# Kernel optimization log

Measured on AMD Instinct MI355X. Metric: run time of the kernel, lower is better.

## Reference

```python
import jax, jax.numpy as jnp
import numpy as np
import math

A = 256            # n_agents == batch rows (epymarl stacks agents along batch)
B = A
OBS = 512          # obs_shape = (input_shape - n_actions) // 2
NA = 64            # n_actions
MSG = 2048         # messages_shape (divisible by A)
H = 1024           # hidden_dim
T = 3              # trajectory_length
TAU = OBS + NA
VD = MSG // A      # per-agent message dim


def setup_inputs() -> dict:
    key = jax.random.key(0)
    keys = iter(jax.random.split(key, 40))
    def lin(o, i):
        w = jax.random.normal(next(keys), (o, i), jnp.float32) * (i ** -0.5)
        return w, jnp.zeros((o,), jnp.float32)
    d = {}
    d["inputs"] = jax.random.normal(next(keys), (B, 2 * OBS + NA + MSG), jnp.float32)
    d["hidden_state"] = jax.random.normal(next(keys), (B, 3 * H), jnp.float32) * 0.1
    for name, o, i in [("pi_fc1", H, OBS + MSG), ("pi_fc2", NA, H),
                       ("fa_fc1", H, OBS), ("fa_fc2", (A - 1) * NA, H),
                       ("fo_fc1", H, NA * A + OBS), ("fo_fc2", OBS, H),
                       ("am_qs", H, MSG), ("am_ks", H, TAU), ("am_vs", VD, TAU)]:
        d[name + "_w"], d[name + "_b"] = lin(o, i)
    for name in ["pi_rnn", "fa_rnn", "fo_rnn"]:
        d[name + "_wih"], d[name + "_bih"] = lin(3 * H, H)
        d[name + "_whh"], d[name + "_bhh"] = lin(3 * H, H)
    return d


def _gru(x, h, wih, whh, bih, bhh):
    gi = x @ wih.T + bih
    gh = h @ whh.T + bhh
    ir, iz, i_n = jnp.split(gi, 3, -1)
    hr, hz, h_n = jnp.split(gh, 3, -1)
    r = jax.nn.sigmoid(ir + hr)
    z = jax.nn.sigmoid(iz + hz)
    n = jnp.tanh(i_n + r * h_n)
    return (1.0 - z) * n + z * h


def reference(inputs, hidden_state,
              pi_fc1_w, pi_fc1_b, pi_fc2_w, pi_fc2_b,
              pi_rnn_wih, pi_rnn_whh, pi_rnn_bih, pi_rnn_bhh,
              fa_fc1_w, fa_fc1_b, fa_fc2_w, fa_fc2_b,
              fa_rnn_wih, fa_rnn_whh, fa_rnn_bih, fa_rnn_bhh,
              fo_fc1_w, fo_fc1_b, fo_fc2_w, fo_fc2_b,
              fo_rnn_wih, fo_rnn_whh, fo_rnn_bih, fo_rnn_bhh,
              am_qs_w, am_qs_b, am_ks_w, am_ks_b, am_vs_w, am_vs_b):
    sg = jax.lax.stop_gradient
    lin = lambda x, w, b: x @ w.T + b
    h_fa = hidden_state[:, :H]
    h_fo = hidden_state[:, H:2 * H]
    h_pi0 = hidden_state[:, -H:]
    obs = inputs[:, :OBS]
    prev_obs = inputs[:, OBS:2 * OBS]
    prev_act = sg(inputs[:, 2 * OBS:2 * OBS + NA])   # .detach() in torch
    prev_msg = inputs[:, -MSG:]

    def pi(o, m, h):
        x = jax.nn.relu(lin(jnp.concatenate([o, m], -1), pi_fc1_w, pi_fc1_b))
        h2 = _gru(x, h, pi_rnn_wih, pi_rnn_whh, pi_rnn_bih, pi_rnn_bhh)
        return lin(h2, pi_fc2_w, pi_fc2_b), h2

    # ---- ImaginedTrajectory rollout (fixed small T, python loop is structural) ----
    o, a, h_pi = prev_obs, prev_act, h_pi0
    observations, actions = [o], [a]
    for _ in range(T - 1):
        x = jax.nn.relu(lin(o, fa_fc1_w, fa_fc1_b))
        h_fa = _gru(x, h_fa, fa_rnn_wih, fa_rnn_whh, fa_rnn_bih, fa_rnn_bhh)
        q = lin(h_fa, fa_fc2_w, fa_fc2_b)                       # [B,(A-1)*NA]
        qs = jax.nn.softmax(q.reshape(B, A - 1, NA), -1)
        # torch stack(qs_out).reshape(orig): scrambles (A-1,B) order, kept faithfully
        fa = jnp.transpose(qs, (1, 0, 2)).reshape(B, (A - 1) * NA)
        x2 = jax.nn.relu(lin(jnp.concatenate([fa, a, o], -1), fo_fc1_w, fo_fc1_b))
        h_fo = _gru(x2, h_fo, fo_rnn_wih, fo_rnn_whh, fo_rnn_bih, fo_rnn_bhh)
        nxt_o = lin(h_fo, fo_fc2_w, fo_fc2_b)
        nxt_a, h_pi = pi(sg(o), sg(prev_msg), sg(h_pi))         # forward_pi detaches inputs
        o, a = nxt_o, nxt_a
        observations.append(o)
        actions.append(a)
    taus = jnp.stack([jnp.concatenate([observations[t], actions[t]], -1)
                      for t in range(T)])                        # [T,B,TAU]

    # ---- AttentionMechanism: batched equivalent of the per-agent python loops ----
    # k rows are indexed j*n_agents + i with batch == n_agents, i.e. k[t, b] here.
    qv = lin(prev_msg, am_qs_w, am_qs_b)                         # [B,H]
    kk = jnp.einsum('tbi,hi->tbh', taus, am_ks_w) + am_ks_b      # [T,B,H]
    vv = jnp.einsum('tbi,vi->tbv', taus, am_vs_w) + am_vs_b      # [T,B,VD]
    alpha = jax.nn.softmax(jnp.einsum('bh,tbh->bt', qv, kk) / math.sqrt(H), -1)
    new_message = jnp.einsum('bt,tbv->bv', alpha, vv)            # [B,VD]

    # cat([msg]*A, 0).reshape(B,-1): each agent receives all agents' messages
    pi_msg = jnp.tile(new_message, (A, 1)).reshape(B, -1)        # [B,MSG]
    action, h_pi_f = pi(obs, pi_msg, h_pi0)                      # uses ORIGINAL h_pi slice
    h_out = jnp.concatenate([h_fa, h_fo, h_pi_f], -1)            # [B,3H]
    q_out = jnp.concatenate([new_message, action], -1)           # [B,VD+NA]
    return q_out, h_out
```

## Files before the change

kernel.cpp:

```cpp
#include <hip/hip_runtime.h>
#include <hip/hip_bf16.h>
#include <math.h>

#define OBS 512
#define MSG 2048
#define TAU 576
#define TAUP 640
#define QN 16320
#define X2W 16896
#define INW 3136
#define PIW 2560

typedef short short8v __attribute__((ext_vector_type(8)));
typedef float f32x4 __attribute__((ext_vector_type(4)));

__device__ inline unsigned short bfbits(float x) {
  __hip_bfloat16 h = __float2bfloat16(x);
  return *reinterpret_cast<unsigned short*>(&h);
}

__device__ inline void gload16(const void* g, void* l) {
  __builtin_amdgcn_global_load_lds((__attribute__((address_space(1))) void*)(g),
                                   (__attribute__((address_space(3))) void*)(l), 16, 0, 0);
}

struct MMSet {
  const __hip_bfloat16* A;
  const float* W;
  const float* bias;
  float* C;
  __hip_bfloat16* Cb;
  int lda, ldw, ldc, ldcb;
};

template<int BM, int ACT, bool ATOMIC, bool DUAL>
__global__ __launch_bounds__(512)
void k_mm(MMSet s0, MMSet s1, int kSteps)
{
  constexpr int AREP = BM / 64;
  __shared__ __hip_bfloat16 As[2][BM * 64];
  __shared__ __hip_bfloat16 Bs[2][64 * 64];
  const MMSet S = (DUAL && blockIdx.z) ? s1 : s0;
  const int tid = threadIdx.x;
  const int lane = tid & 63;
  const int wid = tid >> 6;
  const int m0 = blockIdx.y * BM;
  const int n0 = blockIdx.x * 64;
  const size_t k0 = ATOMIC ? (size_t)blockIdx.z * kSteps * 64 : 0;

  const __hip_bfloat16* Ab = S.A + (size_t)m0 * S.lda + k0;
  const float* Bb = S.W + (size_t)n0 * S.ldw + k0;

  int arow[AREP], acol[AREP], adst[AREP];
#pragma unroll
  for (int r = 0; r < AREP; ++r) {
    int chunk = r * 512 + tid;
    arow[r] = chunk >> 3;
    acol[r] = ((chunk & 7) ^ (arow[r] & 7)) * 8;
    adst[r] = chunk * 8;
  }
  int brow[2], bcol[2], bdst[2];
#pragma unroll
  for (int r = 0; r < 2; ++r) {
    int c = r * 512 + tid;
    brow[r] = c >> 4;
    int g = (c & 15) >> 1, half = c & 1;
    bcol[r] = (c & 15) * 4;
    bdst[r] = brow[r] * 64 + ((g ^ (brow[r] & 7)) << 3) + half * 4;
  }

  const int wr = wid >> 1, wc = wid & 1;
  const int fr = lane & 15, q = lane >> 4;
  const int xm = fr & 7;

  f32x4 acc[AREP][2] = {};
  float4 bv0, bv1;

  auto stageA = [&](int buf, int kt) {
#pragma unroll
    for (int r = 0; r < AREP; ++r)
      gload16(Ab + (size_t)arow[r] * S.lda + kt + acol[r], &As[buf][adst[r]]);
  };
  auto loadB = [&](int kt) {
    bv0 = *(const float4*)(Bb + (size_t)brow[0] * S.ldw + kt + bcol[0]);
    bv1 = *(const float4*)(Bb + (size_t)brow[1] * S.ldw + kt + bcol[1]);
  };
  auto writeB = [&](int buf) {
    ushort4 w0, w1;
    w0.x = bfbits(bv0.x); w0.y = bfbits(bv0.y); w0.z = bfbits(bv0.z); w0.w = bfbits(bv0.w);
    w1.x = bfbits(bv1.x); w1.y = bfbits(bv1.y); w1.z = bfbits(bv1.z); w1.w = bfbits(bv1.w);
    *(ushort4*)&Bs[buf][bdst[0]] = w0;
    *(ushort4*)&Bs[buf][bdst[1]] = w1;
  };

  stageA(0, 0);
  loadB(0);
  writeB(0);
  __syncthreads();

  for (int t = 0; t < kSteps; ++t) {
    const int buf = t & 1;
    if (t + 1 < kSteps) {
      stageA(buf ^ 1, (t + 1) * 64);
      loadB((t + 1) * 64);
    }
    const __hip_bfloat16* Ac = As[buf];
    const __hip_bfloat16* Bc = Bs[buf];
#pragma unroll
    for (int ks = 0; ks < 2; ++ks) {
      const int cc = ks * 4 + q;
      const int co = ((cc ^ xm) << 3);
      short8v b0 = *(const short8v*)&Bc[(wc * 32 +  0 + fr) * 64 + co];
      short8v b1 = *(const short8v*)&Bc[(wc * 32 + 16 + fr) * 64 + co];
#pragma unroll
      for (int i = 0; i < AREP; ++i) {
        short8v a = *(const short8v*)&Ac[(wr * (AREP * 16) + i * 16 + fr) * 64 + co];
        acc[i][0] = __builtin_amdgcn_mfma_f32_16x16x32_bf16(a, b0, acc[i][0], 0, 0, 0);
        acc[i][1] = __builtin_amdgcn_mfma_f32_16x16x32_bf16(a, b1, acc[i][1], 0, 0, 0);
      }
    }
    if (t + 1 < kSteps) writeB(buf ^ 1);
    __syncthreads();
  }

#pragma unroll
  for (int i = 0; i < AREP; ++i) {
    const int mb = m0 + wr * (AREP * 16) + i * 16 + q * 4;
#pragma unroll
    for (int j = 0; j < 2; ++j) {
      const int n = n0 + wc * 32 + j * 16 + fr;
      if (ATOMIC) {
#pragma unroll
        for (int v = 0; v < 4; ++v)
          atomicAdd(&S.C[(size_t)(mb + v) * S.ldc + n], acc[i][j][v]);
      } else {
        const float bb = S.bias[n];
#pragma unroll
        for (int v = 0; v < 4; ++v) {
          float val = acc[i][j][v] + bb;
          if (ACT) val = fmaxf(val, 0.f);
          if (S.C)  S.C[(size_t)(mb + v) * S.ldc + n] = val;
          if (S.Cb) S.Cb[(size_t)(mb + v) * S.ldcb + n] = __float2bfloat16(val);
        }
      }
    }
  }
}

__global__ __launch_bounds__(256)
void k_init(const float* __restrict__ in, const float* __restrict__ hid,
            float* __restrict__ h32a, float* __restrict__ h32o, float* __restrict__ h32p,
            __hip_bfloat16* __restrict__ hba, __hip_bfloat16* __restrict__ hbo,
            __hip_bfloat16* __restrict__ hbp, __hip_bfloat16* __restrict__ hbp0,
            __hip_bfloat16* __restrict__ taus, __hip_bfloat16* __restrict__ msgb)
{
  const int bx = blockIdx.x;
  if (bx < 3072) {
    int idx = bx * 256 + threadIdx.x;
    int b = idx / 3072, c = idx % 3072;
    float v = hid[idx];
    __hip_bfloat16 hb = __float2bfloat16(v);
    int j = c & 1023;
    if (c < 1024)      { h32a[b * 1024 + j] = v; hba[b * 1024 + j] = hb; }
    else if (c < 2048) { h32o[b * 1024 + j] = v; hbo[b * 1024 + j] = hb; }
    else               { h32p[b * 1024 + j] = v; hbp[b * 1024 + j] = hb; hbp0[b * 1024 + j] = hb; }
  } else if (bx < 3072 + 1920) {
    int idx = (bx - 3072) * 256 + threadIdx.x;
    int t = idx / (256 * TAUP);
    int r = (idx / TAUP) % 256;
    int c = idx % TAUP;
    float v = 0.f;
    if (t == 0 && c < TAU)
      v = (c < OBS) ? in[(size_t)r * INW + OBS + c]
                    : in[(size_t)r * INW + 2 * OBS + (c - OBS)];
    taus[idx] = __float2bfloat16(v);
  } else {
    int idx = (bx - 3072 - 1920) * 256 + threadIdx.x;
    int b = idx >> 11, c = idx & 2047;
    msgb[idx] = __float2bfloat16(in[(size_t)b * INW + 1088 + c]);
  }
}

__global__ __launch_bounds__(256)
void k_gru(const float* __restrict__ gi, const float* __restrict__ gh,
           const float* __restrict__ hs, int ldsrc,
           float* __restrict__ hd, int lddst, __hip_bfloat16* __restrict__ hb)
{
  int idx = blockIdx.x * 256 + threadIdx.x;
  int b = idx >> 10, j = idx & 1023;
  float ir = gi[b * 3072 + j];
  float iz = gi[b * 3072 + 1024 + j];
  float in_ = gi[b * 3072 + 2048 + j];
  float hr = gh[b * 3072 + j];
  float hz = gh[b * 3072 + 1024 + j];
  float hn = gh[b * 3072 + 2048 + j];
  float r = 1.f / (1.f + expf(-(ir + hr)));
  float z = 1.f / (1.f + expf(-(iz + hz)));
  float n = tanhf(in_ + r * hn);
  float h = hs[(size_t)b * ldsrc + j];
  float o = (1.f - z) * n + z * h;
  hd[(size_t)b * lddst + j] = o;
  hb[idx] = __float2bfloat16(o);
}

__global__ __launch_bounds__(256)
void k_softmax_scatter(const __hip_bfloat16* __restrict__ q, __hip_bfloat16* __restrict__ x2)
{
  int wid = blockIdx.x * 4 + (threadIdx.x >> 6);
  int lane = threadIdx.x & 63;
  int b = wid / 255, p = wid % 255;
  float v = __bfloat162float(q[(size_t)b * QN + p * 64 + lane]);
  float m = v;
#pragma unroll
  for (int s = 32; s; s >>= 1) m = fmaxf(m, __shfl_xor(m, s));
  float e = expf(v - m);
  float sum = e;
#pragma unroll
  for (int s = 32; s; s >>= 1) sum += __shfl_xor(sum, s);
  float r = e / sum;
  int flat = p * 16384 + b * 64 + lane;
  int bp = flat / QN;
  int j = flat - bp * QN;
  x2[(size_t)bp * X2W + j] = __float2bfloat16(r);
}

__global__ __launch_bounds__(256)
void k_x2_tail(const __hip_bfloat16* __restrict__ taus_t, __hip_bfloat16* __restrict__ x2)
{
  int idx = blockIdx.x * 256 + threadIdx.x;
  int b = idx / TAU, c = idx % TAU;
  if (c < 64)
    x2[(size_t)b * X2W + QN + c] = taus_t[(size_t)b * TAUP + OBS + c];
  else
    x2[(size_t)b * X2W + QN + 64 + (c - 64)] = taus_t[(size_t)b * TAUP + (c - 64)];
}

__global__ __launch_bounds__(256)
void k_concat_pi_loop(const __hip_bfloat16* __restrict__ taus_t,
                      const __hip_bfloat16* __restrict__ msg,
                      __hip_bfloat16* __restrict__ piin)
{
  int idx = blockIdx.x * 256 + threadIdx.x;
  int b = idx / PIW, c = idx % PIW;
  piin[idx] = (c < OBS) ? taus_t[(size_t)b * TAUP + c] : msg[b * MSG + (c - OBS)];
}

__global__ __launch_bounds__(256)
void k_concat_pi_final(const float* __restrict__ in, const float* __restrict__ nm,
                       __hip_bfloat16* __restrict__ piin)
{
  int idx = blockIdx.x * 256 + threadIdx.x;
  int b = idx / PIW, c = idx % PIW;
  float v = (c < OBS) ? in[(size_t)b * INW + c] : nm[c - OBS];
  piin[idx] = __float2bfloat16(v);
}

__global__ __launch_bounds__(256)
void k_fill_bias(float* __restrict__ C, const float* __restrict__ bias)
{
  int idx = blockIdx.x * 256 + threadIdx.x;
  C[idx] = bias[idx & 1023];
}

__global__ __launch_bounds__(256)
void k_relu_cvt(const float* __restrict__ s, __hip_bfloat16* __restrict__ d)
{
  int idx = blockIdx.x * 256 + threadIdx.x;
  d[idx] = __float2bfloat16(fmaxf(s[idx], 0.f));
}

__global__ __launch_bounds__(64)
void k_vv(const __hip_bfloat16* __restrict__ taus, const float* __restrict__ w,
          const float* __restrict__ bias, float* __restrict__ vv)
{
  int row = blockIdx.x;
  int lane = threadIdx.x;
  const __hip_bfloat16* tr = taus + (size_t)row * TAUP;
  for (int v = 0; v < 8; ++v) {
    float s = 0.f;
    for (int k = lane; k < TAU; k += 64) s += __bfloat162float(tr[k]) * w[v * TAU + k];
#pragma unroll
    for (int d = 32; d; d >>= 1) s += __shfl_xor(s, d);
    if (lane == 0) vv[row * 8 + v] = s + bias[v];
  }
}

__global__ __launch_bounds__(64)
void k_attn(const float* __restrict__ qv, const float* __restrict__ kk,
            const float* __restrict__ vv, float* __restrict__ nm,
            float* __restrict__ out_q)
{
  int b = blockIdx.x;
  int lane = threadIdx.x;
  const float* qb = qv + (size_t)b * 1024;
  float s[3];
#pragma unroll
  for (int t = 0; t < 3; ++t) {
    const float* kb = kk + (size_t)(t * 256 + b) * 1024;
    float acc = 0.f;
    for (int h = lane; h < 1024; h += 64) acc += qb[h] * kb[h];
#pragma unroll
    for (int d = 32; d; d >>= 1) acc += __shfl_xor(acc, d);
    s[t] = acc * (1.f / 32.f);
  }
  float m = fmaxf(s[0], fmaxf(s[1], s[2]));
  float e0 = expf(s[0] - m), e1 = expf(s[1] - m), e2 = expf(s[2] - m);
  float inv = 1.f / (e0 + e1 + e2);
  float a0 = e0 * inv, a1 = e1 * inv, a2 = e2 * inv;
  if (lane < 8) {
    float v = a0 * vv[(0 * 256 + b) * 8 + lane]
            + a1 * vv[(1 * 256 + b) * 8 + lane]
            + a2 * vv[(2 * 256 + b) * 8 + lane];
    nm[b * 8 + lane] = v;
    out_q[b * 72 + lane] = v;
  }
}

__global__ __launch_bounds__(256)
void k_copy_hout(const float* __restrict__ hfa, const float* __restrict__ hfo,
                 float* __restrict__ hout)
{
  int idx = blockIdx.x * 256 + threadIdx.x;
  int b = idx / 2048, c = idx % 2048;
  float v = (c < 1024) ? hfa[b * 1024 + c] : hfo[b * 1024 + (c - 1024)];
  hout[(size_t)b * 3072 + c] = v;
}

extern "C" void kernel_launch(void* const* d_in, const int* in_sizes, int n_in,
                              void* d_out_v, int out_size, void* d_ws, size_t ws_size,
                              hipStream_t stream)
{
  const float* inputs   = (const float*)d_in[0];
  const float* hidden   = (const float*)d_in[1];
  const float* pi_fc1_w = (const float*)d_in[2];
  const float* pi_fc1_b = (const float*)d_in[3];
  const float* pi_fc2_w = (const float*)d_in[4];
  const float* pi_fc2_b = (const float*)d_in[5];
  const float* fa_fc1_w = (const float*)d_in[6];
  const float* fa_fc1_b = (const float*)d_in[7];
  const float* fa_fc2_w = (const float*)d_in[8];
  const float* fa_fc2_b = (const float*)d_in[9];
  const float* fo_fc1_w = (const float*)d_in[10];
  const float* fo_fc1_b = (const float*)d_in[11];
  const float* fo_fc2_w = (const float*)d_in[12];
  const float* fo_fc2_b = (const float*)d_in[13];
  const float* am_qs_w  = (const float*)d_in[14];
  const float* am_qs_b  = (const float*)d_in[15];
  const float* am_ks_w  = (const float*)d_in[16];
  const float* am_ks_b  = (const float*)d_in[17];
  const float* am_vs_w  = (const float*)d_in[18];
  const float* am_vs_b  = (const float*)d_in[19];
  const float* pi_wih   = (const float*)d_in[20];
  const float* pi_bih   = (const float*)d_in[21];
  const float* pi_whh   = (const float*)d_in[22];
  const float* pi_bhh   = (const float*)d_in[23];
  const float* fa_wih   = (const float*)d_in[24];
  const float* fa_bih   = (const float*)d_in[25];
  const float* fa_whh   = (const float*)d_in[26];
  const float* fa_bhh   = (const float*)d_in[27];
  const float* fo_wih   = (const float*)d_in[28];
  const float* fo_bih   = (const float*)d_in[29];
  const float* fo_whh   = (const float*)d_in[30];
  const float* fo_bhh   = (const float*)d_in[31];

  float* out = (float*)d_out_v;
  char* p = (char*)d_ws;
  auto alloc = [&](size_t bytes) { void* r = p; p += (bytes + 255) & ~(size_t)255; return r; };
  typedef __hip_bfloat16 bf;

  bf* HFAB = (bf*)alloc((size_t)256 * 1024 * 2);
  bf* HFOB = (bf*)alloc((size_t)256 * 1024 * 2);
  bf* HPIB = (bf*)alloc((size_t)256 * 1024 * 2);
  bf* HPI0B = (bf*)alloc((size_t)256 * 1024 * 2);
  bf* XBUFB = (bf*)alloc((size_t)256 * 1024 * 2);
  bf* TAUSB = (bf*)alloc((size_t)3 * 256 * TAUP * 2);
  bf* X2B  = (bf*)alloc((size_t)256 * X2W * 2);
  bf* PIINB = (bf*)alloc((size_t)256 * PIW * 2);
  bf* MSGB = (bf*)alloc((size_t)256 * MSG * 2);
  bf* QBUFB = (bf*)alloc((size_t)256 * QN * 2);
  float* HFA32 = (float*)alloc((size_t)256 * 1024 * 4);
  float* HFO32 = (float*)alloc((size_t)256 * 1024 * 4);
  float* HPI32 = (float*)alloc((size_t)256 * 1024 * 4);
  float* XBUF32 = (float*)alloc((size_t)256 * 1024 * 4);
  float* GI = (float*)alloc((size_t)256 * 3072 * 4);
  float* GH = (float*)alloc((size_t)256 * 3072 * 4);
  float* QV = (float*)alloc((size_t)256 * 1024 * 4);
  float* KK = (float*)alloc((size_t)768 * 1024 * 4);
  float* VV = (float*)alloc((size_t)768 * 8 * 4);
  float* NM = (float*)alloc((size_t)2048 * 4);

  auto mset = [&](const bf* A, int lda, const float* W, int ldw, const float* bias,
                  float* C, int ldc, bf* Cb, int ldcb) {
    MMSet s; s.A = A; s.W = W; s.bias = bias; s.C = C; s.Cb = Cb;
    s.lda = lda; s.ldw = ldw; s.ldc = ldc; s.ldcb = ldcb; return s;
  };
  auto mm256 = [&](MMSet a, int M, int N, int K) {
    dim3 g(N / 64, M / 256, 1);
    k_mm<256, 0, false, false><<<g, 512, 0, stream>>>(a, a, K / 64);
  };
  auto mm128 = [&](MMSet a, int M, int N, int K) {
    dim3 g(N / 64, M / 128, 1);
    k_mm<128, 0, false, false><<<g, 512, 0, stream>>>(a, a, K / 64);
  };
  auto mm64 = [&](MMSet a, int N, int K, int act) {
    dim3 g(N / 64, 4, 1);
    if (act) k_mm<64, 1, false, false><<<g, 512, 0, stream>>>(a, a, K / 64);
    else     k_mm<64, 0, false, false><<<g, 512, 0, stream>>>(a, a, K / 64);
  };
  auto mmDual = [&](MMSet a, MMSet b, int N, int K) {
    dim3 g(N / 64, 2, 2);
    k_mm<128, 0, false, true><<<g, 512, 0, stream>>>(a, b, K / 64);
  };

  k_init<<<3072 + 1920 + 2048, 256, 0, stream>>>(inputs, hidden,
      HFA32, HFO32, HPI32, HFAB, HFOB, HPIB, HPI0B, TAUSB, MSGB);

  for (int t = 0; t < 2; ++t) {
    bf* taus_t = TAUSB + (size_t)t * 256 * TAUP;
    bf* taus_n = TAUSB + (size_t)(t + 1) * 256 * TAUP;
    mm64(mset(taus_t, TAUP, fa_fc1_w, 512, fa_fc1_b, nullptr, 0, XBUFB, 1024), 1024, 512, 1);
    mmDual(mset(XBUFB, 1024, fa_wih, 1024, fa_bih, GI, 3072, nullptr, 0),
           mset(HFAB, 1024, fa_whh, 1024, fa_bhh, GH, 3072, nullptr, 0), 3072, 1024);
    k_gru<<<1024, 256, 0, stream>>>(GI, GH, HFA32, 1024, HFA32, 1024, HFAB);
    mm256(mset(HFAB, 1024, fa_fc2_w, 1024, fa_fc2_b, nullptr, 0, QBUFB, QN), 256, QN, 1024);
    k_x2_tail<<<576, 256, 0, stream>>>(taus_t, X2B);
    k_softmax_scatter<<<16320, 256, 0, stream>>>(QBUFB, X2B);
    k_fill_bias<<<1024, 256, 0, stream>>>(XBUF32, fo_fc1_b);
    {
      dim3 g(16, 1, 12);
      MMSet s = mset(X2B, X2W, fo_fc1_w, X2W, fo_fc1_b, XBUF32, 1024, nullptr, 0);
      k_mm<256, 0, true, false><<<g, 512, 0, stream>>>(s, s, 22);
    }
    k_relu_cvt<<<1024, 256, 0, stream>>>(XBUF32, XBUFB);
    mmDual(mset(XBUFB, 1024, fo_wih, 1024, fo_bih, GI, 3072, nullptr, 0),
           mset(HFOB, 1024, fo_whh, 1024, fo_bhh, GH, 3072, nullptr, 0), 3072, 1024);
    k_gru<<<1024, 256, 0, stream>>>(GI, GH, HFO32, 1024, HFO32, 1024, HFOB);
    mm64(mset(HFOB, 1024, fo_fc2_w, 1024, fo_fc2_b, nullptr, 0, taus_n, TAUP), 512, 1024, 0);
    k_concat_pi_loop<<<2560, 256, 0, stream>>>(taus_t, MSGB, PIINB);
    mm64(mset(PIINB, PIW, pi_fc1_w, PIW, pi_fc1_b, nullptr, 0, XBUFB, 1024), 1024, PIW, 1);
    mmDual(mset(XBUFB, 1024, pi_wih, 1024, pi_bih, GI, 3072, nullptr, 0),
           mset(HPIB, 1024, pi_whh, 1024, pi_bhh, GH, 3072, nullptr, 0), 3072, 1024);
    k_gru<<<1024, 256, 0, stream>>>(GI, GH, HPI32, 1024, HPI32, 1024, HPIB);
    mm64(mset(HPIB, 1024, pi_fc2_w, 1024, pi_fc2_b, nullptr, 0, taus_n + OBS, TAUP), 64, 1024, 0);
  }

  mm64(mset(MSGB, MSG, am_qs_w, MSG, am_qs_b, QV, 1024, nullptr, 0), 1024, 2048, 0);
  mm128(mset(TAUSB, TAUP, am_ks_w, TAU, am_ks_b, KK, 1024, nullptr, 0), 768, 1024, TAU);
  k_vv<<<768, 64, 0, stream>>>(TAUSB, am_vs_w, am_vs_b, VV);
  k_attn<<<256, 64, 0, stream>>>(QV, KK, VV, NM, out);

  k_concat_pi_final<<<2560, 256, 0, stream>>>(inputs, NM, PIINB);
  mm64(mset(PIINB, PIW, pi_fc1_w, PIW, pi_fc1_b, nullptr, 0, XBUFB, 1024), 1024, PIW, 1);
  mmDual(mset(XBUFB, 1024, pi_wih, 1024, pi_bih, GI, 3072, nullptr, 0),
         mset(HPI0B, 1024, pi_whh, 1024, pi_bhh, GH, 3072, nullptr, 0), 3072, 1024);
  k_gru<<<1024, 256, 0, stream>>>(GI, GH, hidden + 2048, 3072,
                                  out + 256 * 72 + 2048, 3072, HPIB);
  mm64(mset(HPIB, 1024, pi_fc2_w, 1024, pi_fc2_b, out + 8, 72, nullptr, 0), 64, 1024, 0);
  k_copy_hout<<<2048, 256, 0, stream>>>(HFA32, HFO32, out + 256 * 72);
  (void)in_sizes; (void)n_in; (void)out_size; (void)ws_size;
}
```

Measured before the change: 611.9 us.

## Triple-buffer GEMM pipeline, enlarge tiles, fold fo_fc1 bias fill into init

The GEMM main loop moves from a double-buffered to a triple-buffered LDS pipeline. Loads run two k-steps ahead, with explicit lgkmcnt waits, barriers and raised wave priority around the MFMA block, to hide global load latency. Several launches switch to larger M tiles (the dual GRU GEMMs to BM=256, pi_fc1 and am_qs to BM=128, am_ks to BM=256), which cuts weight re-reads but leaves fewer blocks in the grid. The separate bias-fill kernel for the atomic fo_fc1 accumulation is dropped and both per-step buffers are pre-filled in the init kernel, at the cost of one extra 1 MB buffer and 50% more LDS per block.

After: 801.7 us. +31.0%, slower.

```diff
diff --git a/kernel.cpp b/kernel.cpp
--- a/kernel.cpp
+++ b/kernel.cpp
@@ -24,6 +24,13 @@
                                    (__attribute__((address_space(3))) void*)(l), 16, 0, 0);
 }
 
+__device__ inline void bar_lgkm() {
+  __builtin_amdgcn_sched_barrier(0);
+  asm volatile("s_waitcnt lgkmcnt(0)" ::: "memory");
+  __builtin_amdgcn_s_barrier();
+  __builtin_amdgcn_sched_barrier(0);
+}
+
 struct MMSet {
   const __hip_bfloat16* A;
   const float* W;
@@ -38,8 +45,8 @@
 void k_mm(MMSet s0, MMSet s1, int kSteps)
 {
   constexpr int AREP = BM / 64;
-  __shared__ __hip_bfloat16 As[2][BM * 64];
-  __shared__ __hip_bfloat16 Bs[2][64 * 64];
+  __shared__ __hip_bfloat16 As[3][BM * 64];
+  __shared__ __hip_bfloat16 Bs[3][64 * 64];
   const MMSet S = (DUAL && blockIdx.z) ? s1 : s0;
   const int tid = threadIdx.x;
   const int lane = tid & 63;
@@ -74,38 +81,53 @@
   const int xm = fr & 7;
 
   f32x4 acc[AREP][2] = {};
-  float4 bv0, bv1;
+  float4 p0a, p0b, p1a, p1b;
 
   auto stageA = [&](int buf, int kt) {
 #pragma unroll
     for (int r = 0; r < AREP; ++r)
       gload16(Ab + (size_t)arow[r] * S.lda + kt + acol[r], &As[buf][adst[r]]);
   };
-  auto loadB = [&](int kt) {
-    bv0 = *(const float4*)(Bb + (size_t)brow[0] * S.ldw + kt + bcol[0]);
-    bv1 = *(const float4*)(Bb + (size_t)brow[1] * S.ldw + kt + bcol[1]);
-  };
-  auto writeB = [&](int buf) {
+  auto loadB0 = [&](int kt) {
+    p0a = *(const float4*)(Bb + (size_t)brow[0] * S.ldw + kt + bcol[0]);
+    p0b = *(const float4*)(Bb + (size_t)brow[1] * S.ldw + kt + bcol[1]);
+  };
+  auto loadB1 = [&](int kt) {
+    p1a = *(const float4*)(Bb + (size_t)brow[0] * S.ldw + kt + bcol[0]);
+    p1b = *(const float4*)(Bb + (size_t)brow[1] * S.ldw + kt + bcol[1]);
+  };
+  auto writeB0 = [&](int buf) {
     ushort4 w0, w1;
-    w0.x = bfbits(bv0.x); w0.y = bfbits(bv0.y); w0.z = bfbits(bv0.z); w0.w = bfbits(bv0.w);
-    w1.x = bfbits(bv1.x); w1.y = bfbits(bv1.y); w1.z = bfbits(bv1.z); w1.w = bfbits(bv1.w);
+    w0.x = bfbits(p0a.x); w0.y = bfbits(p0a.y); w0.z = bfbits(p0a.z); w0.w = bfbits(p0a.w);
+    w1.x = bfbits(p0b.x); w1.y = bfbits(p0b.y); w1.z = bfbits(p0b.z); w1.w = bfbits(p0b.w);
     *(ushort4*)&Bs[buf][bdst[0]] = w0;
     *(ushort4*)&Bs[buf][bdst[1]] = w1;
   };
-
-  stageA(0, 0);
-  loadB(0);
-  writeB(0);
-  __syncthreads();
+  auto writeB1 = [&](int buf) {
+    ushort4 w0, w1;
+    w0.x = bfbits(p1a.x); w0.y = bfbits(p1a.y); w0.z = bfbits(p1a.z); w0.w = bfbits(p1a.w);
+    w1.x = bfbits(p1b.x); w1.y = bfbits(p1b.y); w1.z = bfbits(p1b.z); w1.w = bfbits(p1b.w);
+    *(ushort4*)&Bs[buf][bdst[0]] = w0;
+    *(ushort4*)&Bs[buf][bdst[1]] = w1;
+  };
+
+  stageA(0, 0); loadB0(0);
+  if (kSteps > 1) { stageA(1, 64); loadB1(64); }
+  writeB0(0);
 
   for (int t = 0; t < kSteps; ++t) {
-    const int buf = t & 1;
+    bar_lgkm();
+    if (t + 2 < kSteps) {
+      stageA((t + 2) % 3, (t + 2) * 64);
+      if (t & 1) loadB1((t + 2) * 64); else loadB0((t + 2) * 64);
+    }
     if (t + 1 < kSteps) {
-      stageA(buf ^ 1, (t + 1) * 64);
-      loadB((t + 1) * 64);
+      if (t & 1) writeB0((t + 1) % 3); else writeB1((t + 1) % 3);
     }
-    const __hip_bfloat16* Ac = As[buf];
-    const __hip_bfloat16* Bc = Bs[buf];
+    bar_lgkm();
+    const __hip_bfloat16* Ac = As[t % 3];
+    const __hip_bfloat16* Bc = Bs[t % 3];
+    __builtin_amdgcn_s_setprio(1);
 #pragma unroll
     for (int ks = 0; ks < 2; ++ks) {
       const int cc = ks * 4 + q;
@@ -119,8 +141,7 @@
         acc[i][1] = __builtin_amdgcn_mfma_f32_16x16x32_bf16(a, b1, acc[i][1], 0, 0, 0);
       }
     }
-    if (t + 1 < kSteps) writeB(buf ^ 1);
-    __syncthreads();
+    __builtin_amdgcn_s_setprio(0);
   }
 
 #pragma unroll
@@ -152,7 +173,8 @@
             float* __restrict__ h32a, float* __restrict__ h32o, float* __restrict__ h32p,
             __hip_bfloat16* __restrict__ hba, __hip_bfloat16* __restrict__ hbo,
             __hip_bfloat16* __restrict__ hbp, __hip_bfloat16* __restrict__ hbp0,
-            __hip_bfloat16* __restrict__ taus, __hip_bfloat16* __restrict__ msgb)
+            __hip_bfloat16* __restrict__ taus, __hip_bfloat16* __restrict__ msgb,
+            const float* __restrict__ fo1b, float* __restrict__ xb0, float* __restrict__ xb1)
 {
   const int bx = blockIdx.x;
   if (bx < 3072) {
@@ -174,10 +196,14 @@
       v = (c < OBS) ? in[(size_t)r * INW + OBS + c]
                     : in[(size_t)r * INW + 2 * OBS + (c - OBS)];
     taus[idx] = __float2bfloat16(v);
-  } else {
+  } else if (bx < 3072 + 1920 + 2048) {
     int idx = (bx - 3072 - 1920) * 256 + threadIdx.x;
     int b = idx >> 11, c = idx & 2047;
     msgb[idx] = __float2bfloat16(in[(size_t)b * INW + 1088 + c]);
+  } else {
+    int idx = (bx - 3072 - 1920 - 2048) * 256 + threadIdx.x;
+    float v = fo1b[idx & 1023];
+    xb0[idx] = v; xb1[idx] = v;
   }
 }
 
@@ -253,13 +279,6 @@
   int b = idx / PIW, c = idx % PIW;
   float v = (c < OBS) ? in[(size_t)b * INW + c] : nm[c - OBS];
   piin[idx] = __float2bfloat16(v);
-}
-
-__global__ __launch_bounds__(256)
-void k_fill_bias(float* __restrict__ C, const float* __restrict__ bias)
-{
-  int idx = blockIdx.x * 256 + threadIdx.x;
-  C[idx] = bias[idx & 1023];
 }
 
 __global__ __launch_bounds__(256)
@@ -381,7 +400,8 @@
   float* HFA32 = (float*)alloc((size_t)256 * 1024 * 4);
   float* HFO32 = (float*)alloc((size_t)256 * 1024 * 4);
   float* HPI32 = (float*)alloc((size_t)256 * 1024 * 4);
-  float* XBUF32 = (float*)alloc((size_t)256 * 1024 * 4);
+  float* XBUF32A = (float*)alloc((size_t)256 * 1024 * 4);
+  float* XBUF32B = (float*)alloc((size_t)256 * 1024 * 4);
   float* GI = (float*)alloc((size_t)256 * 3072 * 4);
   float* GH = (float*)alloc((size_t)256 * 3072 * 4);
   float* QV = (float*)alloc((size_t)256 * 1024 * 4);
@@ -398,9 +418,10 @@
     dim3 g(N / 64, M / 256, 1);
     k_mm<256, 0, false, false><<<g, 512, 0, stream>>>(a, a, K / 64);
   };
-  auto mm128 = [&](MMSet a, int M, int N, int K) {
+  auto mm128 = [&](MMSet a, int M, int N, int K, int act) {
     dim3 g(N / 64, M / 128, 1);
-    k_mm<128, 0, false, false><<<g, 512, 0, stream>>>(a, a, K / 64);
+    if (act) k_mm<128, 1, false, false><<<g, 512, 0, stream>>>(a, a, K / 64);
+    else     k_mm<128, 0, false, false><<<g, 512, 0, stream>>>(a, a, K / 64);
   };
   auto mm64 = [&](MMSet a, int N, int K, int act) {
     dim3 g(N / 64, 4, 1);
@@ -408,16 +429,18 @@
     else     k_mm<64, 0, false, false><<<g, 512, 0, stream>>>(a, a, K / 64);
   };
   auto mmDual = [&](MMSet a, MMSet b, int N, int K) {
-    dim3 g(N / 64, 2, 2);
-    k_mm<128, 0, false, true><<<g, 512, 0, stream>>>(a, b, K / 64);
-  };
-
-  k_init<<<3072 + 1920 + 2048, 256, 0, stream>>>(inputs, hidden,
-      HFA32, HFO32, HPI32, HFAB, HFOB, HPIB, HPI0B, TAUSB, MSGB);
+    dim3 g(N / 64, 1, 2);
+    k_mm<256, 0, false, true><<<g, 512, 0, stream>>>(a, b, K / 64);
+  };
+
+  k_init<<<3072 + 1920 + 2048 + 1024, 256, 0, stream>>>(inputs, hidden,
+      HFA32, HFO32, HPI32, HFAB, HFOB, HPIB, HPI0B, TAUSB, MSGB,
+      fo_fc1_b, XBUF32A, XBUF32B);
 
   for (int t = 0; t < 2; ++t) {
     bf* taus_t = TAUSB + (size_t)t * 256 * TAUP;
     bf* taus_n = TAUSB + (size_t)(t + 1) * 256 * TAUP;
+    float* xb32 = t ? XBUF32B : XBUF32A;
     mm64(mset(taus_t, TAUP, fa_fc1_w, 512, fa_fc1_b, nullptr, 0, XBUFB, 1024), 1024, 512, 1);
     mmDual(mset(XBUFB, 1024, fa_wih, 1024, fa_bih, GI, 3072, nullptr, 0),
            mset(HFAB, 1024, fa_whh, 1024, fa_bhh, GH, 3072, nullptr, 0), 3072, 1024);
@@ -425,32 +448,31 @@
     mm256(mset(HFAB, 1024, fa_fc2_w, 1024, fa_fc2_b, nullptr, 0, QBUFB, QN), 256, QN, 1024);
     k_x2_tail<<<576, 256, 0, stream>>>(taus_t, X2B);
     k_softmax_scatter<<<16320, 256, 0, stream>>>(QBUFB, X2B);
-    k_fill_bias<<<1024, 256, 0, stream>>>(XBUF32, fo_fc1_b);
     {
       dim3 g(16, 1, 12);
-      MMSet s = mset(X2B, X2W, fo_fc1_w, X2W, fo_fc1_b, XBUF32, 1024, nullptr, 0);
+      MMSet s = mset(X2B, X2W, fo_fc1_w, X2W, fo_fc1_b, xb32, 1024, nullptr, 0);
       k_mm<256, 0, true, false><<<g, 512, 0, stream>>>(s, s, 22);
     }
-    k_relu_cvt<<<1024, 256, 0, stream>>>(XBUF32, XBUFB);
+    k_relu_cvt<<<1024, 256, 0, stream>>>(xb32, XBUFB);
     mmDual(mset(XBUFB, 1024, fo_wih, 1024, fo_bih, GI, 3072, nullptr, 0),
            mset(HFOB, 1024, fo_whh, 1024, fo_bhh, GH, 3072, nullptr, 0), 3072, 1024);
     k_gru<<<1024, 256, 0, stream>>>(GI, GH, HFO32, 1024, HFO32, 1024, HFOB);
     mm64(mset(HFOB, 1024, fo_fc2_w, 1024, fo_fc2_b, nullptr, 0, taus_n, TAUP), 512, 1024, 0);
     k_concat_pi_loop<<<2560, 256, 0, stream>>>(taus_t, MSGB, PIINB);
-    mm64(mset(PIINB, PIW, pi_fc1_w, PIW, pi_fc1_b, nullptr, 0, XBUFB, 1024), 1024, PIW, 1);
+    mm128(mset(PIINB, PIW, pi_fc1_w, PIW, pi_fc1_b, nullptr, 0, XBUFB, 1024), 256, 1024, PIW, 1);
     mmDual(mset(XBUFB, 1024, pi_wih, 1024, pi_bih, GI, 3072, nullptr, 0),
            mset(HPIB, 1024, pi_whh, 1024, pi_bhh, GH, 3072, nullptr, 0), 3072, 1024);
     k_gru<<<1024, 256, 0, stream>>>(GI, GH, HPI32, 1024, HPI32, 1024, HPIB);
     mm64(mset(HPIB, 1024, pi_fc2_w, 1024, pi_fc2_b, nullptr, 0, taus_n + OBS, TAUP), 64, 1024, 0);
   }
 
-  mm64(mset(MSGB, MSG, am_qs_w, MSG, am_qs_b, QV, 1024, nullptr, 0), 1024, 2048, 0);
-  mm128(mset(TAUSB, TAUP, am_ks_w, TAU, am_ks_b, KK, 1024, nullptr, 0), 768, 1024, TAU);
+  mm128(mset(MSGB, MSG, am_qs_w, MSG, am_qs_b, QV, 1024, nullptr, 0), 256, 1024, 2048, 0);
+  mm256(mset(TAUSB, TAUP, am_ks_w, TAU, am_ks_b, KK, 1024, nullptr, 0), 768, 1024, TAU);
   k_vv<<<768, 64, 0, stream>>>(TAUSB, am_vs_w, am_vs_b, VV);
   k_attn<<<256, 64, 0, stream>>>(QV, KK, VV, NM, out);
 
   k_concat_pi_final<<<2560, 256, 0, stream>>>(inputs, NM, PIINB);
-  mm64(mset(PIINB, PIW, pi_fc1_w, PIW, pi_fc1_b, nullptr, 0, XBUFB, 1024), 1024, PIW, 1);
+  mm128(mset(PIINB, PIW, pi_fc1_w, PIW, pi_fc1_b, nullptr, 0, XBUFB, 1024), 256, 1024, PIW, 1);
   mmDual(mset(XBUFB, 1024, pi_wih, 1024, pi_bih, GI, 3072, nullptr, 0),
          mset(HPI0B, 1024, pi_whh, 1024, pi_bhh, GH, 3072, nullptr, 0), 3072, 1024);
   k_gru<<<1024, 256, 0, stream>>>(GI, GH, hidden + 2048, 3072,
```

## Use uniform 64x64 GEMM tiles, split-K pi_fc1, and fold bias fills into init

Applied to the files above, without the earlier changes.

Replaces the variable-BM 512-thread GEMM kernel with a single 64x64-tile, 256-thread kernel so every GEMM launches more blocks for the small M=256 problems. The pi_fc1 GEMMs now use split-K with atomic accumulation into bias-prefilled fp32 buffers, followed by a ReLU/convert pass. The separate bias-fill kernels are folded into the init kernel, using distinct buffers per use. This trades more blocks and atomics, plus more reloads of A and weight tiles, for better CU occupancy on the skinny matmuls.

After: 637.0 us. +4.1%, slower.

```diff
diff --git a/kernel.cpp b/kernel.cpp
--- a/kernel.cpp
+++ b/kernel.cpp
@@ -13,10 +13,17 @@
 
 typedef short short8v __attribute__((ext_vector_type(8)));
 typedef float f32x4 __attribute__((ext_vector_type(4)));
+typedef __hip_bfloat16 bf;
 
 __device__ inline unsigned short bfbits(float x) {
-  __hip_bfloat16 h = __float2bfloat16(x);
+  bf h = __float2bfloat16(x);
   return *reinterpret_cast<unsigned short*>(&h);
+}
+
+__device__ inline ushort4 cvtf4(float4 v) {
+  ushort4 r;
+  r.x = bfbits(v.x); r.y = bfbits(v.y); r.z = bfbits(v.z); r.w = bfbits(v.w);
+  return r;
 }
 
 __device__ inline void gload16(const void* g, void* l) {
@@ -25,44 +32,43 @@
 }
 
 struct MMSet {
-  const __hip_bfloat16* A;
+  const bf* A;
   const float* W;
   const float* bias;
   float* C;
-  __hip_bfloat16* Cb;
+  bf* Cb;
   int lda, ldw, ldc, ldcb;
 };
 
-template<int BM, int ACT, bool ATOMIC, bool DUAL>
-__global__ __launch_bounds__(512)
+template<int ACT, bool ATOMIC, bool DUAL>
+__global__ __launch_bounds__(256)
 void k_mm(MMSet s0, MMSet s1, int kSteps)
 {
-  constexpr int AREP = BM / 64;
-  __shared__ __hip_bfloat16 As[2][BM * 64];
-  __shared__ __hip_bfloat16 Bs[2][64 * 64];
+  __shared__ bf As[2][64 * 64];
+  __shared__ bf Bs[2][64 * 64];
   const MMSet S = (DUAL && blockIdx.z) ? s1 : s0;
   const int tid = threadIdx.x;
   const int lane = tid & 63;
   const int wid = tid >> 6;
-  const int m0 = blockIdx.y * BM;
+  const int m0 = blockIdx.y * 64;
   const int n0 = blockIdx.x * 64;
   const size_t k0 = ATOMIC ? (size_t)blockIdx.z * kSteps * 64 : 0;
 
-  const __hip_bfloat16* Ab = S.A + (size_t)m0 * S.lda + k0;
+  const bf* Ab = S.A + (size_t)m0 * S.lda + k0;
   const float* Bb = S.W + (size_t)n0 * S.ldw + k0;
 
-  int arow[AREP], acol[AREP], adst[AREP];
-#pragma unroll
-  for (int r = 0; r < AREP; ++r) {
-    int chunk = r * 512 + tid;
+  int arow[2], acol[2], adst[2];
+#pragma unroll
+  for (int r = 0; r < 2; ++r) {
+    int chunk = r * 256 + tid;
     arow[r] = chunk >> 3;
     acol[r] = ((chunk & 7) ^ (arow[r] & 7)) * 8;
     adst[r] = chunk * 8;
   }
-  int brow[2], bcol[2], bdst[2];
-#pragma unroll
-  for (int r = 0; r < 2; ++r) {
-    int c = r * 512 + tid;
+  int brow[4], bcol[4], bdst[4];
+#pragma unroll
+  for (int r = 0; r < 4; ++r) {
+    int c = r * 256 + tid;
     brow[r] = c >> 4;
     int g = (c & 15) >> 1, half = c & 1;
     bcol[r] = (c & 15) * 4;
@@ -73,24 +79,25 @@
   const int fr = lane & 15, q = lane >> 4;
   const int xm = fr & 7;
 
-  f32x4 acc[AREP][2] = {};
-  float4 bv0, bv1;
+  f32x4 acc00 = {}, acc01 = {}, acc10 = {}, acc11 = {};
+  float4 w0, w1, w2, w3;
 
   auto stageA = [&](int buf, int kt) {
 #pragma unroll
-    for (int r = 0; r < AREP; ++r)
+    for (int r = 0; r < 2; ++r)
       gload16(Ab + (size_t)arow[r] * S.lda + kt + acol[r], &As[buf][adst[r]]);
   };
   auto loadB = [&](int kt) {
-    bv0 = *(const float4*)(Bb + (size_t)brow[0] * S.ldw + kt + bcol[0]);
-    bv1 = *(const float4*)(Bb + (size_t)brow[1] * S.ldw + kt + bcol[1]);
+    w0 = *(const float4*)(Bb + (size_t)brow[0] * S.ldw + kt + bcol[0]);
+    w1 = *(const float4*)(Bb + (size_t)brow[1] * S.ldw + kt + bcol[1]);
+    w2 = *(const float4*)(Bb + (size_t)brow[2] * S.ldw + kt + bcol[2]);
+    w3 = *(const float4*)(Bb + (size_t)brow[3] * S.ldw + kt + bcol[3]);
   };
   auto writeB = [&](int buf) {
-    ushort4 w0, w1;
-    w0.x = bfbits(bv0.x); w0.y = bfbits(bv0.y); w0.z = bfbits(bv0.z); w0.w = bfbits(bv0.w);
-    w1.x = bfbits(bv1.x); w1.y = bfbits(bv1.y); w1.z = bfbits(bv1.z); w1.w = bfbits(bv1.w);
-    *(ushort4*)&Bs[buf][bdst[0]] = w0;
-    *(ushort4*)&Bs[buf][bdst[1]] = w1;
+    *(ushort4*)&Bs[buf][bdst[0]] = cvtf4(w0);
+    *(ushort4*)&Bs[buf][bdst[1]] = cvtf4(w1);
+    *(ushort4*)&Bs[buf][bdst[2]] = cvtf4(w2);
+    *(ushort4*)&Bs[buf][bdst[3]] = cvtf4(w3);
   };
 
   stageA(0, 0);
@@ -104,44 +111,56 @@
       stageA(buf ^ 1, (t + 1) * 64);
       loadB((t + 1) * 64);
     }
-    const __hip_bfloat16* Ac = As[buf];
-    const __hip_bfloat16* Bc = Bs[buf];
+    const bf* Ac = As[buf];
+    const bf* Bc = Bs[buf];
 #pragma unroll
     for (int ks = 0; ks < 2; ++ks) {
       const int cc = ks * 4 + q;
       const int co = ((cc ^ xm) << 3);
+      short8v a0 = *(const short8v*)&Ac[(wr * 32 +  0 + fr) * 64 + co];
+      short8v a1 = *(const short8v*)&Ac[(wr * 32 + 16 + fr) * 64 + co];
       short8v b0 = *(const short8v*)&Bc[(wc * 32 +  0 + fr) * 64 + co];
       short8v b1 = *(const short8v*)&Bc[(wc * 32 + 16 + fr) * 64 + co];
-#pragma unroll
-      for (int i = 0; i < AREP; ++i) {
-        short8v a = *(const short8v*)&Ac[(wr * (AREP * 16) + i * 16 + fr) * 64 + co];
-        acc[i][0] = __builtin_amdgcn_mfma_f32_16x16x32_bf16(a, b0, acc[i][0], 0, 0, 0);
-        acc[i][1] = __builtin_amdgcn_mfma_f32_16x16x32_bf16(a, b1, acc[i][1], 0, 0, 0);
-      }
+      acc00 = __builtin_amdgcn_mfma_f32_16x16x32_bf16(a0, b0, acc00, 0, 0, 0);
+      acc01 = __builtin_amdgcn_mfma_f32_16x16x32_bf16(a0, b1, acc01, 0, 0, 0);
+      acc10 = __builtin_amdgcn_mfma_f32_16x16x32_bf16(a1, b0, acc10, 0, 0, 0);
+      acc11 = __builtin_amdgcn_mfma_f32_16x16x32_bf16(a1, b1, acc11, 0, 0, 0);
     }
     if (t + 1 < kSteps) writeB(buf ^ 1);
     __syncthreads();
   }
 
-#pragma unroll
-  for (int i = 0; i < AREP; ++i) {
-    const int mb = m0 + wr * (AREP * 16) + i * 16 + q * 4;
-#pragma unroll
-    for (int j = 0; j < 2; ++j) {
-      const int n = n0 + wc * 32 + j * 16 + fr;
-      if (ATOMIC) {
-#pragma unroll
-        for (int v = 0; v < 4; ++v)
-          atomicAdd(&S.C[(size_t)(mb + v) * S.ldc + n], acc[i][j][v]);
-      } else {
-        const float bb = S.bias[n];
-#pragma unroll
-        for (int v = 0; v < 4; ++v) {
-          float val = acc[i][j][v] + bb;
-          if (ACT) val = fmaxf(val, 0.f);
-          if (S.C)  S.C[(size_t)(mb + v) * S.ldc + n] = val;
-          if (S.Cb) S.Cb[(size_t)(mb + v) * S.ldcb + n] = __float2bfloat16(val);
-        }
+  const int mb0 = m0 + wr * 32 + q * 4;
+  const int mb1 = mb0 + 16;
+  const int nc0 = n0 + wc * 32 + fr;
+  const int nc1 = nc0 + 16;
+  if (ATOMIC) {
+#pragma unroll
+    for (int v = 0; v < 4; ++v) {
+      atomicAdd(&S.C[(size_t)(mb0 + v) * S.ldc + nc0], acc00[v]);
+      atomicAdd(&S.C[(size_t)(mb0 + v) * S.ldc + nc1], acc01[v]);
+      atomicAdd(&S.C[(size_t)(mb1 + v) * S.ldc + nc0], acc10[v]);
+      atomicAdd(&S.C[(size_t)(mb1 + v) * S.ldc + nc1], acc11[v]);
+    }
+  } else {
+    const float bb0 = S.bias[nc0], bb1 = S.bias[nc1];
+#pragma unroll
+    for (int v = 0; v < 4; ++v) {
+      float v00 = acc00[v] + bb0, v01 = acc01[v] + bb1;
+      float v10 = acc10[v] + bb0, v11 = acc11[v] + bb1;
+      if (ACT) { v00 = fmaxf(v00, 0.f); v01 = fmaxf(v01, 0.f);
+                 v10 = fmaxf(v10, 0.f); v11 = fmaxf(v11, 0.f); }
+      if (S.C) {
+        S.C[(size_t)(mb0 + v) * S.ldc + nc0] = v00;
+        S.C[(size_t)(mb0 + v) * S.ldc + nc1] = v01;
+        S.C[(size_t)(mb1 + v) * S.ldc + nc0] = v10;
+        S.C[(size_t)(mb1 + v) * S.ldc + nc1] = v11;
+      }
+      if (S.Cb) {
+        S.Cb[(size_t)(mb0 + v) * S.ldcb + nc0] = __float2bfloat16(v00);
+        S.Cb[(size_t)(mb0 + v) * S.ldcb + nc1] = __float2bfloat16(v01);
+        S.Cb[(size_t)(mb1 + v) * S.ldcb + nc0] = __float2bfloat16(v10);
+        S.Cb[(size_t)(mb1 + v) * S.ldcb + nc1] = __float2bfloat16(v11);
       }
     }
   }
@@ -150,16 +169,19 @@
 __global__ __launch_bounds__(256)
 void k_init(const float* __restrict__ in, const float* __restrict__ hid,
             float* __restrict__ h32a, float* __restrict__ h32o, float* __restrict__ h32p,
-            __hip_bfloat16* __restrict__ hba, __hip_bfloat16* __restrict__ hbo,
-            __hip_bfloat16* __restrict__ hbp, __hip_bfloat16* __restrict__ hbp0,
-            __hip_bfloat16* __restrict__ taus, __hip_bfloat16* __restrict__ msgb)
+            bf* __restrict__ hba, bf* __restrict__ hbo,
+            bf* __restrict__ hbp, bf* __restrict__ hbp0,
+            bf* __restrict__ taus, bf* __restrict__ msgb,
+            const float* __restrict__ fo1b, float* __restrict__ xf0, float* __restrict__ xf1,
+            const float* __restrict__ pi1b, float* __restrict__ xp0,
+            float* __restrict__ xp1, float* __restrict__ xp2)
 {
   const int bx = blockIdx.x;
   if (bx < 3072) {
     int idx = bx * 256 + threadIdx.x;
     int b = idx / 3072, c = idx % 3072;
     float v = hid[idx];
-    __hip_bfloat16 hb = __float2bfloat16(v);
+    bf hb = __float2bfloat16(v);
     int j = c & 1023;
     if (c < 1024)      { h32a[b * 1024 + j] = v; hba[b * 1024 + j] = hb; }
     else if (c < 2048) { h32o[b * 1024 + j] = v; hbo[b * 1024 + j] = hb; }
@@ -174,17 +196,25 @@
       v = (c < OBS) ? in[(size_t)r * INW + OBS + c]
                     : in[(size_t)r * INW + 2 * OBS + (c - OBS)];
     taus[idx] = __float2bfloat16(v);
-  } else {
+  } else if (bx < 3072 + 1920 + 2048) {
     int idx = (bx - 3072 - 1920) * 256 + threadIdx.x;
     int b = idx >> 11, c = idx & 2047;
     msgb[idx] = __float2bfloat16(in[(size_t)b * INW + 1088 + c]);
+  } else if (bx < 3072 + 1920 + 2048 + 1024) {
+    int idx = (bx - 3072 - 1920 - 2048) * 256 + threadIdx.x;
+    float v = fo1b[idx & 1023];
+    xf0[idx] = v; xf1[idx] = v;
+  } else {
+    int idx = (bx - 3072 - 1920 - 2048 - 1024) * 256 + threadIdx.x;
+    float v = pi1b[idx & 1023];
+    xp0[idx] = v; xp1[idx] = v; xp2[idx] = v;
   }
 }
 
 __global__ __launch_bounds__(256)
 void k_gru(const float* __restrict__ gi, const float* __restrict__ gh,
            const float* __restrict__ hs, int ldsrc,
-           float* __restrict__ hd, int lddst, __hip_bfloat16* __restrict__ hb)
+           float* __restrict__ hd, int lddst, bf* __restrict__ hb)
 {
   int idx = blockIdx.x * 256 + threadIdx.x;
   int b = idx >> 10, j = idx & 1023;
@@ -204,7 +234,7 @@
 }
 
 __global__ __launch_bounds__(256)
-void k_softmax_scatter(const __hip_bfloat16* __restrict__ q, __hip_bfloat16* __restrict__ x2)
+void k_softmax_scatter(const bf* __restrict__ q, bf* __restrict__ x2)
 {
   int wid = blockIdx.x * 4 + (threadIdx.x >> 6);
   int lane = threadIdx.x & 63;
@@ -225,7 +255,7 @@
 }
 
 __global__ __launch_bounds__(256)
-void k_x2_tail(const __hip_bfloat16* __restrict__ taus_t, __hip_bfloat16* __restrict__ x2)
+void k_x2_tail(const bf* __restrict__ taus_t, bf* __restrict__ x2)
 {
   int idx = blockIdx.x * 256 + threadIdx.x;
   int b = idx / TAU, c = idx % TAU;
@@ -236,9 +266,8 @@
 }
 
 __global__ __launch_bounds__(256)
-void k_concat_pi_loop(const __hip_bfloat16* __restrict__ taus_t,
-                      const __hip_bfloat16* __restrict__ msg,
-                      __hip_bfloat16* __restrict__ piin)
+void k_concat_pi_loop(const bf* __restrict__ taus_t, const bf* __restrict__ msg,
+                      bf* __restrict__ piin)
 {
   int idx = blockIdx.x * 256 + threadIdx.x;
   int b = idx / PIW, c = idx % PIW;
@@ -247,7 +276,7 @@
 
 __global__ __launch_bounds__(256)
 void k_concat_pi_final(const float* __restrict__ in, const float* __restrict__ nm,
-                       __hip_bfloat16* __restrict__ piin)
+                       bf* __restrict__ piin)
 {
   int idx = blockIdx.x * 256 + threadIdx.x;
   int b = idx / PIW, c = idx % PIW;
@@ -256,26 +285,19 @@
 }
 
 __global__ __launch_bounds__(256)
-void k_fill_bias(float* __restrict__ C, const float* __restrict__ bias)
-{
-  int idx = blockIdx.x * 256 + threadIdx.x;
-  C[idx] = bias[idx & 1023];
-}
-
-__global__ __launch_bounds__(256)
-void k_relu_cvt(const float* __restrict__ s, __hip_bfloat16* __restrict__ d)
+void k_relu_cvt(const float* __restrict__ s, bf* __restrict__ d)
 {
   int idx = blockIdx.x * 256 + threadIdx.x;
   d[idx] = __float2bfloat16(fmaxf(s[idx], 0.f));
 }
 
 __global__ __launch_bounds__(64)
-void k_vv(const __hip_bfloat16* __restrict__ taus, const float* __restrict__ w,
+void k_vv(const bf* __restrict__ taus, const float* __restrict__ w,
           const float* __restrict__ bias, float* __restrict__ vv)
 {
   int row = blockIdx.x;
   int lane = threadIdx.x;
-  const __hip_bfloat16* tr = taus + (size_t)row * TAUP;
+  const bf* tr = taus + (size_t)row * TAUP;
   for (int v = 0; v < 8; ++v) {
     float s = 0.f;
     for (int k = lane; k < TAU; k += 64) s += __bfloat162float(tr[k]) * w[v * TAU + k];
@@ -366,7 +388,6 @@
   float* out = (float*)d_out_v;
   char* p = (char*)d_ws;
   auto alloc = [&](size_t bytes) { void* r = p; p += (bytes + 255) & ~(size_t)255; return r; };
-  typedef __hip_bfloat16 bf;
 
   bf* HFAB = (bf*)alloc((size_t)256 * 1024 * 2);
   bf* HFOB = (bf*)alloc((size_t)256 * 1024 * 2);
@@ -381,7 +402,11 @@
   float* HFA32 = (float*)alloc((size_t)256 * 1024 * 4);
   float* HFO32 = (float*)alloc((size_t)256 * 1024 * 4);
   float* HPI32 = (float*)alloc((size_t)256 * 1024 * 4);
-  float* XBUF32 = (float*)alloc((size_t)256 * 1024 * 4);
+  float* XF32A = (float*)alloc((size_t)256 * 1024 * 4);
+  float* XF32B = (float*)alloc((size_t)256 * 1024 * 4);
+  float* XP32A = (float*)alloc((size_t)256 * 1024 * 4);
+  float* XP32B = (float*)alloc((size_t)256 * 1024 * 4);
+  float* XP32C = (float*)alloc((size_t)256 * 1024 * 4);
   float* GI = (float*)alloc((size_t)256 * 3072 * 4);
   float* GH = (float*)alloc((size_t)256 * 3072 * 4);
   float* QV = (float*)alloc((size_t)256 * 1024 * 4);
@@ -394,68 +419,66 @@
     MMSet s; s.A = A; s.W = W; s.bias = bias; s.C = C; s.Cb = Cb;
     s.lda = lda; s.ldw = ldw; s.ldc = ldc; s.ldcb = ldcb; return s;
   };
-  auto mm256 = [&](MMSet a, int M, int N, int K) {
-    dim3 g(N / 64, M / 256, 1);
-    k_mm<256, 0, false, false><<<g, 512, 0, stream>>>(a, a, K / 64);
-  };
-  auto mm128 = [&](MMSet a, int M, int N, int K) {
-    dim3 g(N / 64, M / 128, 1);
-    k_mm<128, 0, false, false><<<g, 512, 0, stream>>>(a, a, K / 64);
-  };
-  auto mm64 = [&](MMSet a, int N, int K, int act) {
-    dim3 g(N / 64, 4, 1);
-    if (act) k_mm<64, 1, false, false><<<g, 512, 0, stream>>>(a, a, K / 64);
-    else     k_mm<64, 0, false, false><<<g, 512, 0, stream>>>(a, a, K / 64);
+  auto mm = [&](MMSet a, int M, int N, int K, int act) {
+    dim3 g(N / 64, M / 64, 1);
+    if (act) k_mm<1, false, false><<<g, 256, 0, stream>>>(a, a, K / 64);
+    else     k_mm<0, false, false><<<g, 256, 0, stream>>>(a, a, K / 64);
+  };
+  auto mmAtomic = [&](const bf* A, int lda, const float* W, int ldw,
+                      float* C, int M, int N, int K, int z) {
+    MMSet s = mset(A, lda, W, ldw, nullptr, C, N, nullptr, 0);
+    dim3 g(N / 64, M / 64, z);
+    k_mm<0, true, false><<<g, 256, 0, stream>>>(s, s, K / (64 * z));
   };
   auto mmDual = [&](MMSet a, MMSet b, int N, int K) {
-    dim3 g(N / 64, 2, 2);
-    k_mm<128, 0, false, true><<<g, 512, 0, stream>>>(a, b, K / 64);
-  };
-
-  k_init<<<3072 + 1920 + 2048, 256, 0, stream>>>(inputs, hidden,
-      HFA32, HFO32, HPI32, HFAB, HFOB, HPIB, HPI0B, TAUSB, MSGB);
+    dim3 g(N / 64, 4, 2);
+    k_mm<0, false, true><<<g, 256, 0, stream>>>(a, b, K / 64);
+  };
+
+  k_init<<<3072 + 1920 + 2048 + 1024 + 1024, 256, 0, stream>>>(inputs, hidden,
+      HFA32, HFO32, HPI32, HFAB, HFOB, HPIB, HPI0B, TAUSB, MSGB,
+      fo_fc1_b, XF32A, XF32B, pi_fc1_b, XP32A, XP32B, XP32C);
 
   for (int t = 0; t < 2; ++t) {
     bf* taus_t = TAUSB + (size_t)t * 256 * TAUP;
     bf* taus_n = TAUSB + (size_t)(t + 1) * 256 * TAUP;
-    mm64(mset(taus_t, TAUP, fa_fc1_w, 512, fa_fc1_b, nullptr, 0, XBUFB, 1024), 1024, 512, 1);
+    float* xf32 = t ? XF32B : XF32A;
+    float* xp32 = t ? XP32B : XP32A;
+    mm(mset(taus_t, TAUP, fa_fc1_w, 512, fa_fc1_b, nullptr, 0, XBUFB, 1024), 256, 1024, 512, 1);
     mmDual(mset(XBUFB, 1024, fa_wih, 1024, fa_bih, GI, 3072, nullptr, 0),
            mset(HFAB, 1024, fa_whh, 1024, fa_bhh, GH, 3072, nullptr, 0), 3072, 1024);
     k_gru<<<1024, 256, 0, stream>>>(GI, GH, HFA32, 1024, HFA32, 1024, HFAB);
-    mm256(mset(HFAB, 1024, fa_fc2_w, 1024, fa_fc2_b, nullptr, 0, QBUFB, QN), 256, QN, 1024);
+    mm(mset(HFAB, 1024, fa_fc2_w, 1024, fa_fc2_b, nullptr, 0, QBUFB, QN), 256, QN, 1024, 0);
     k_x2_tail<<<576, 256, 0, stream>>>(taus_t, X2B);
     k_softmax_scatter<<<16320, 256, 0, stream>>>(QBUFB, X2B);
-    k_fill_bias<<<1024, 256, 0, stream>>>(XBUF32, fo_fc1_b);
-    {
-      dim3 g(16, 1, 12);
-      MMSet s = mset(X2B, X2W, fo_fc1_w, X2W, fo_fc1_b, XBUF32, 1024, nullptr, 0);
-      k_mm<256, 0, true, false><<<g, 512, 0, stream>>>(s, s, 22);
-    }
-    k_relu_cvt<<<1024, 256, 0, stream>>>(XBUF32, XBUFB);
+    mmAtomic(X2B, X2W, fo_fc1_w, X2W, xf32, 256, 1024, X2W, 12);
+    k_relu_cvt<<<1024, 256, 0, stream>>>(xf32, XBUFB);
     mmDual(mset(XBUFB, 1024, fo_wih, 1024, fo_bih, GI, 3072, nullptr, 0),
            mset(HFOB, 1024, fo_whh, 1024, fo_bhh, GH, 3072, nullptr, 0), 3072, 1024);
     k_gru<<<1024, 256, 0, stream>>>(GI, GH, HFO32, 1024, HFO32, 1024, HFOB);
-    mm64(mset(HFOB, 1024, fo_fc2_w, 1024, fo_fc2_b, nullptr, 0, taus_n, TAUP), 512, 1024, 0);
+    mm(mset(HFOB, 1024, fo_fc2_w, 1024, fo_fc2_b, nullptr, 0, taus_n, TAUP), 256, 512, 1024, 0);
     k_concat_pi_loop<<<2560, 256, 0, stream>>>(taus_t, MSGB, PIINB);
-    mm64(mset(PIINB, PIW, pi_fc1_w, PIW, pi_fc1_b, nullptr, 0, XBUFB, 1024), 1024, PIW, 1);
+    mmAtomic(PIINB, PIW, pi_fc1_w, PIW, xp32, 256, 1024, PIW, 4);
+    k_relu_cvt<<<1024, 256, 0, stream>>>(xp32, XBUFB);
     mmDual(mset(XBUFB, 1024, pi_wih, 1024, pi_bih, GI, 3072, nullptr, 0),
            mset(HPIB, 1024, pi_whh, 1024, pi_bhh, GH, 3072, nullptr, 0), 3072, 1024);
     k_gru<<<1024, 256, 0, stream>>>(GI, GH, HPI32, 1024, HPI32, 1024, HPIB);
-    mm64(mset(HPIB, 1024, pi_fc2_w, 1024, pi_fc2_b, nullptr, 0, taus_n + OBS, TAUP), 64, 1024, 0);
-  }
-
-  mm64(mset(MSGB, MSG, am_qs_w, MSG, am_qs_b, QV, 1024, nullptr, 0), 1024, 2048, 0);
-  mm128(mset(TAUSB, TAUP, am_ks_w, TAU, am_ks_b, KK, 1024, nullptr, 0), 768, 1024, TAU);
+    mm(mset(HPIB, 1024, pi_fc2_w, 1024, pi_fc2_b, nullptr, 0, taus_n + OBS, TAUP), 256, 64, 1024, 0);
+  }
+
+  mm(mset(MSGB, MSG, am_qs_w, MSG, am_qs_b, QV, 1024, nullptr, 0), 256, 1024, 2048, 0);
+  mm(mset(TAUSB, TAUP, am_ks_w, TAU, am_ks_b, KK, 1024, nullptr, 0), 768, 1024, TAU, 0);
   k_vv<<<768, 64, 0, stream>>>(TAUSB, am_vs_w, am_vs_b, VV);
   k_attn<<<256, 64, 0, stream>>>(QV, KK, VV, NM, out);
 
   k_concat_pi_final<<<2560, 256, 0, stream>>>(inputs, NM, PIINB);
-  mm64(mset(PIINB, PIW, pi_fc1_w, PIW, pi_fc1_b, nullptr, 0, XBUFB, 1024), 1024, PIW, 1);
+  mmAtomic(PIINB, PIW, pi_fc1_w, PIW, XP32C, 256, 1024, PIW, 4);
+  k_relu_cvt<<<1024, 256, 0, stream>>>(XP32C, XBUFB);
   mmDual(mset(XBUFB, 1024, pi_wih, 1024, pi_bih, GI, 3072, nullptr, 0),
          mset(HPI0B, 1024, pi_whh, 1024, pi_bhh, GH, 3072, nullptr, 0), 3072, 1024);
   k_gru<<<1024, 256, 0, stream>>>(GI, GH, hidden + 2048, 3072,
                                   out + 256 * 72 + 2048, 3072, HPIB);
-  mm64(mset(HPIB, 1024, pi_fc2_w, 1024, pi_fc2_b, out + 8, 72, nullptr, 0), 64, 1024, 0);
+  mm(mset(HPIB, 1024, pi_fc2_w, 1024, pi_fc2_b, out + 8, 72, nullptr, 0), 256, 64, 1024, 0);
   k_copy_hout<<<2048, 256, 0, stream>>>(HFA32, HFO32, out + 256 * 72);
   (void)in_sizes; (void)n_in; (void)out_size; (void)ws_size;
 }
```
